# Kernel optimization log

Measured on AMD Instinct MI355X. Metric: run time of the kernel, lower is better.

## Reference

```python
import jax, jax.numpy as jnp
import numpy as np

N = 100_000      # nodes
E = 1_600_000    # edges (before self loops)
F_IN = 128       # dataset.num_node_features
H = 64           # hidden_channels
C = 10           # dataset.num_classes
B = 128          # graphs in batch
NEG_SLOPE = 0.2  # GATConv default


def setup_inputs() -> dict:
    key = jax.random.key(0)
    ks = jax.random.split(key, 16)
    s = 0.05
    x = jax.random.normal(ks[0], (N, F_IN), jnp.float32)
    edge_index = jax.random.randint(ks[1], (2, E), 0, N, dtype=jnp.int32).astype(jnp.int64)
    batch = jnp.sort(jax.random.randint(ks[2], (N,), 0, B, dtype=jnp.int32)).astype(jnp.int64)
    inp = {"x": x, "edge_index": edge_index, "batch": batch}
    # GATConv params: lin weight [out,in], att_src/att_dst [out], bias [out]
    dims = [(H, F_IN), (H, H), (H, H)]
    for i, (o, fi) in enumerate(dims, start=1):
        k = jax.random.split(ks[2 + i], 4)
        inp[f"W{i}"] = jax.random.normal(k[0], (o, fi), jnp.float32) * s
        inp[f"a_src{i}"] = jax.random.normal(k[1], (o,), jnp.float32) * s
        inp[f"a_dst{i}"] = jax.random.normal(k[2], (o,), jnp.float32) * s
        inp[f"b{i}"] = jax.random.normal(k[3], (o,), jnp.float32) * s
    inp["W_lin"] = jax.random.normal(ks[8], (C, H), jnp.float32) * s
    inp["b_lin"] = jax.random.normal(ks[9], (C,), jnp.float32) * s
    return inp


def gat_conv(x, src, dst, W, a_src, a_dst, b):
    # x: [N,Fin]; src/dst: [E+N] (self loops appended)
    h = x @ W.T                      # [N,H]
    e_src = h @ a_src                # [N] per-node src score
    e_dst = h @ a_dst                # [N] per-node dst score
    e = jax.nn.leaky_relu(e_src[src] + e_dst[dst], NEG_SLOPE)  # [E+N]
    # segment softmax over incoming edges of each dst node
    m = jax.ops.segment_max(e, dst, num_segments=N)
    ex = jnp.exp(e - m[dst])
    denom = jax.ops.segment_sum(ex, dst, num_segments=N)
    alpha = ex / denom[dst]          # [E+N]
    out = jax.ops.segment_sum(h[src] * alpha[:, None], dst, num_segments=N)
    return out + b


def reference(x, edge_index, batch, W1, a_src1, a_dst1, b1,
              W2, a_src2, a_dst2, b2, W3, a_src3, a_dst3, b3,
              W_lin, b_lin):
    loops = jnp.arange(N, dtype=edge_index.dtype)
    src = jnp.concatenate([edge_index[0], loops])
    dst = jnp.concatenate([edge_index[1], loops])
    h = jax.nn.relu(gat_conv(x, src, dst, W1, a_src1, a_dst1, b1))
    h = jax.nn.relu(gat_conv(h, src, dst, W2, a_src2, a_dst2, b2))
    h = gat_conv(h, src, dst, W3, a_src3, a_dst3, b3)
    # global mean pool over graphs
    sums = jax.ops.segment_sum(h, batch, num_segments=B)          # [B,H]
    cnt = jax.ops.segment_sum(jnp.ones((N,), h.dtype), batch, num_segments=B)
    pooled = sums / jnp.maximum(cnt, 1.0)[:, None]
    # dropout is identity in eval mode
    return pooled @ W_lin.T + b_lin   # [B,C]
```

## Files before the change

kernel.cpp:

```cpp
#include <hip/hip_runtime.h>
#include <hip/hip_bf16.h>

#define NN 100000
#define EE 1600000
#define ETOT 1700000
#define FIN1 128
#define HD 64
#define NC 10
#define NB 128
#define NEG 0.2f
#define LOG2E 1.44269504f

#define NBKT 196
#define BCAP 10240
#define BLKE 4096
#define ABLOCKS ((ETOT + BLKE - 1) / BLKE)
#define GBLOCKS ((NN + 63) / 64)


static constexpr size_t OFF_HA   = 0;
static constexpr size_t OFF_HB   = (size_t)NN * HD;
static constexpr size_t OFF_ESA  = (size_t)NN * HD * 2;
static constexpr size_t OFF_EDA  = OFF_ESA + (size_t)NN * 4;
static constexpr size_t OFF_ESB  = OFF_EDA + (size_t)NN * 4;
static constexpr size_t OFF_EDB  = OFF_ESB + (size_t)NN * 4;
static constexpr size_t OFF_ROW  = OFF_EDB + (size_t)NN * 4;
static constexpr size_t OFF_CSR  = OFF_ROW + (size_t)(NN + 4) * 4;
static constexpr size_t OFF_GC   = OFF_CSR + (size_t)ETOT * 4;
static constexpr size_t OFF_POOL = OFF_GC + 1024;
static constexpr size_t OFF_BKT  = OFF_POOL + (size_t)NB * HD * 4;

typedef __attribute__((ext_vector_type(8))) short short8;
typedef __attribute__((ext_vector_type(4))) float floatx4;
typedef __attribute__((ext_vector_type(2))) float floatx2;

__device__ __forceinline__ unsigned short f2bf(float f) {
  unsigned u = __float_as_uint(f);
  if ((u & 0x7F800000u) == 0x7F800000u) return (unsigned short)(u >> 16);
  return (unsigned short)((u + 0x7FFFu + ((u >> 16) & 1u)) >> 16);
}
__device__ __forceinline__ unsigned pk2(float a, float b) {
  return (unsigned)f2bf(a) | ((unsigned)f2bf(b) << 16);
}

#if __has_builtin(__builtin_amdgcn_cvt_pk_fp8_f32) && __has_builtin(__builtin_amdgcn_cvt_pk_f32_fp8)
#define HW_FP8 1
#endif
__device__ __forceinline__ unsigned enc1_fp8(float f) {
  _Float16 hf = (_Float16)f;
  unsigned short b = __builtin_bit_cast(unsigned short, hf);
  unsigned s = ((unsigned)b >> 8) & 0x80u;
  int mag = b & 0x7fff;
  if (mag < 0x2380) return s;
  int r = mag + 0x3F + ((mag >> 7) & 1);
  int m = (r >> 7) - 64;
  if (m > 0x7E) m = 0x7E;
  return s | (unsigned)m;
}
__device__ __forceinline__ unsigned pack4_fp8(float a, float b, float c, float d) {
#ifdef HW_FP8
  int w = __builtin_amdgcn_cvt_pk_fp8_f32(a, b, 0, false);
  w = __builtin_amdgcn_cvt_pk_fp8_f32(c, d, w, true);
  return (unsigned)w;
#else
  return enc1_fp8(a) | (enc1_fp8(b) << 8) | (enc1_fp8(c) << 16) | (enc1_fp8(d) << 24);
#endif
}
__device__ __forceinline__ float dec1_fp8(unsigned byte) {
  unsigned short hb = (unsigned short)(((byte & 0x80u) << 8) | ((byte & 0x7fu) << 7));
  _Float16 hf = __builtin_bit_cast(_Float16, hb);
  return (float)hf * 256.0f;
}
template <bool HI>
__device__ __forceinline__ floatx2 unpk2_fp8(unsigned w) {
#ifdef HW_FP8
  return __builtin_amdgcn_cvt_pk_f32_fp8((int)w, HI);
#else
  unsigned s = HI ? (w >> 16) : w;
  floatx2 r; r.x = dec1_fp8(s & 0xffu); r.y = dec1_fp8((s >> 8) & 0xffu);
  return r;
#endif
}

__device__ __forceinline__ void acc16(float* acc, float w, uint4 u) {
  floatx2 f0 = unpk2_fp8<false>(u.x), f1 = unpk2_fp8<true>(u.x);
  floatx2 f2 = unpk2_fp8<false>(u.y), f3 = unpk2_fp8<true>(u.y);
  floatx2 f4 = unpk2_fp8<false>(u.z), f5 = unpk2_fp8<true>(u.z);
  floatx2 f6 = unpk2_fp8<false>(u.w), f7 = unpk2_fp8<true>(u.w);
  acc[0]  = fmaf(w, f0.x, acc[0]);  acc[1]  = fmaf(w, f0.y, acc[1]);
  acc[2]  = fmaf(w, f1.x, acc[2]);  acc[3]  = fmaf(w, f1.y, acc[3]);
  acc[4]  = fmaf(w, f2.x, acc[4]);  acc[5]  = fmaf(w, f2.y, acc[5]);
  acc[6]  = fmaf(w, f3.x, acc[6]);  acc[7]  = fmaf(w, f3.y, acc[7]);
  acc[8]  = fmaf(w, f4.x, acc[8]);  acc[9]  = fmaf(w, f4.y, acc[9]);
  acc[10] = fmaf(w, f5.x, acc[10]); acc[11] = fmaf(w, f5.y, acc[11]);
  acc[12] = fmaf(w, f6.x, acc[12]); acc[13] = fmaf(w, f6.y, acc[13]);
  acc[14] = fmaf(w, f7.x, acc[14]); acc[15] = fmaf(w, f7.y, acc[15]);
}

__device__ __forceinline__ float aggregate_node(
    int n, int fl, const int* __restrict__ rowptr, const int* __restrict__ csr,
    const float* __restrict__ esIn, const float* __restrict__ edIn,
    const uint4* __restrict__ h16, float* acc) {
#pragma unroll
  for (int j = 0; j < 16; j++) acc[j] = 0.f;
  const float edn = edIn[n];
  const int row = rowptr[n];
  const int end = rowptr[n + 1];
  const int endm1 = end - 1;
  float den = 0.f;
  int idx0 = row + fl;
  int s_cur = csr[(idx0 < end) ? idx0 : endm1];
  float ev_cur = esIn[s_cur];
  for (int i = row; i < end; i += 4) {
    int inext = i + 4;
    int s_nxt = s_cur;
    if (inext < end) {
      int idn = inext + fl;
      s_nxt = csr[(idn < end) ? idn : endm1];
    }
    float ev_nxt = esIn[s_nxt];
    float e = ev_cur + edn;
    e = fmaxf(e, NEG * e);
    float w = exp2f(e);
    w = (i + fl < end) ? w : 0.f;
    den += w;
    int s0 = __shfl(s_cur, 0, 4), s1 = __shfl(s_cur, 1, 4);
    int s2 = __shfl(s_cur, 2, 4), s3 = __shfl(s_cur, 3, 4);
    float w0 = __shfl(w, 0, 4), w1 = __shfl(w, 1, 4);
    float w2 = __shfl(w, 2, 4), w3 = __shfl(w, 3, 4);
    uint4 u0 = h16[s0 * 4 + fl];
    uint4 u1 = h16[s1 * 4 + fl];
    uint4 u2 = h16[s2 * 4 + fl];
    uint4 u3 = h16[s3 * 4 + fl];
    acc16(acc, w0, u0);
    acc16(acc, w1, u1);
    acc16(acc, w2, u2);
    acc16(acc, w3, u3);
    s_cur = s_nxt;
    ev_cur = ev_nxt;
  }
  den += __shfl_xor(den, 1, 4);
  den += __shfl_xor(den, 2, 4);
  return 1.0f / den;
}

__device__ __forceinline__ void bucketA_body(
    int bid, const int* __restrict__ EI, unsigned* __restrict__ bucketed,
    int* __restrict__ gcur, char* smem) {
  unsigned* stage = (unsigned*)smem;
  unsigned short* sb = (unsigned short*)(smem + BLKE * 4);
  int* cnt  = (int*)(smem + BLKE * 4 + BLKE * 2);
  int* lofs = cnt + NBKT;
  int* base = lofs + NBKT;
  int* sc   = base + NBKT;
  const int t = threadIdx.x;
  const long long start = (long long)bid * BLKE;
  long long rem = (long long)ETOT - start;
  const int V = (rem < BLKE) ? (int)rem : BLKE;
  unsigned pk[BLKE / 256];
  short bk[BLKE / 256];
  for (int i = t; i < NBKT; i += 256) cnt[i] = 0;
  __syncthreads();
#pragma unroll
  for (int j = 0; j < BLKE / 256; j++) {
    long long k = start + t + 256 * j;
    bk[j] = -1;
    if (k < ETOT) {
      int s, d;
      if (k < EE) { s = EI[k]; d = EI[(long long)EE + k]; }
      else        { s = d = (int)(k - EE); }
      int b = d >> 9;
      pk[j] = ((unsigned)s << 9) | (unsigned)(d & 511);
      bk[j] = (short)b;
      atomicAdd(&cnt[b], 1);
    }
  }
  __syncthreads();
  int own = (t < NBKT) ? cnt[t] : 0;
  sc[t] = own;
  __syncthreads();
  for (int off = 1; off < 256; off <<= 1) {
    int add = (t >= off) ? sc[t - off] : 0;
    __syncthreads();
    sc[t] += add;
    __syncthreads();
  }
  if (t < NBKT) {
    lofs[t] = sc[t] - own;
    base[t] = (own > 0) ? atomicAdd(&gcur[t], own) : 0;
    cnt[t] = 0;
  }
  __syncthreads();
#pragma unroll
  for (int j = 0; j < BLKE / 256; j++) {
    if (bk[j] >= 0) {
      int b = bk[j];
      int p = lofs[b] + atomicAdd(&cnt[b], 1);
      stage[p] = pk[j];
      sb[p] = (unsigned short)b;
    }
  }
  __syncthreads();
  for (int i = t; i < V; i += 256) {
    int b = sb[i];
    int pos = base[b] + (i - lofs[b]);
    if (pos < BCAP) bucketed[(long long)b * BCAP + pos] = stage[i];
  }
}

__device__ __forceinline__ void gemm1_body(
    int bid, const float* __restrict__ X, const float* __restrict__ W,
    const float* __restrict__ As, const float* __restrict__ Ad,
    unsigned* __restrict__ hout, float* __restrict__ es, float* __restrict__ ed,
    char* smem) {
  constexpr int K = FIN1, RW = K / 2;
  unsigned* Xw = (unsigned*)smem;
  unsigned* Ww = (unsigned*)(smem + 16384);
  const int t = threadIdx.x;
  const int nodeBase = bid * 64;

  for (int i4 = t * 4; i4 < 64 * K; i4 += 1024) {
    int node = i4 >> 7, k = i4 & (K - 1);
    float4 v = make_float4(0.f, 0.f, 0.f, 0.f);
    if (nodeBase + node < NN)
      v = *(const float4*)(X + ((long long)(nodeBase + node) << 7) + k);
    uint2 p = make_uint2(pk2(v.x, v.y), pk2(v.z, v.w));
    int kw = k >> 1;
    *(uint2*)&Xw[node * RW + (kw ^ ((node & 7) << 2))] = p;
  }
  for (int i4 = t * 4; i4 < 64 * K; i4 += 1024) {
    int f = i4 >> 7, k = i4 & (K - 1);
    float4 v = *(const float4*)(W + ((long long)f << 7) + k);
    uint2 p = make_uint2(pk2(v.x, v.y), pk2(v.z, v.w));
    int kw = k >> 1;
    *(uint2*)&Ww[f * RW + (kw ^ ((f & 7) << 2))] = p;
  }
  __syncthreads();

  const int w = t >> 6, l = t & 63, m = l & 15, q = l >> 4;
  const int nodeLoc = 16 * w + m;
  const int sxa = (nodeLoc & 7) << 2;
  floatx4 acc[4];
#pragma unroll
  for (int nt = 0; nt < 4; nt++) acc[nt] = (floatx4){0.f, 0.f, 0.f, 0.f};
#pragma unroll
  for (int kc = 0; kc < K; kc += 32) {
    const int kcw = (kc >> 1) + 4 * q;
    short8 af = *(const short8*)&Xw[nodeLoc * RW + (kcw ^ sxa)];
#pragma unroll
    for (int nt = 0; nt < 4; nt++) {
      int f = 16 * nt + m;
      short8 bf = *(const short8*)&Ww[f * RW + (kcw ^ ((f & 7) << 2))];
      acc[nt] = __builtin_amdgcn_mfma_f32_16x16x32_bf16(af, bf, acc[nt], 0, 0, 0);
    }
  }
  float asv[4], adv[4];
#pragma unroll
  for (int nt = 0; nt < 4; nt++) { asv[nt] = As[16 * nt + m]; adv[nt] = Ad[16 * nt + m]; }
#pragma unroll
  for (int r = 0; r < 4; r++) {
    float ss = 0.f, sd2 = 0.f;
#pragma unroll
    for (int nt = 0; nt < 4; nt++) {
      ss = fmaf(acc[nt][r], asv[nt], ss);
      sd2 = fmaf(acc[nt][r], adv[nt], sd2);
    }
#pragma unroll
    for (int off = 1; off < 16; off <<= 1) {
      ss += __shfl_xor(ss, off);
      sd2 += __shfl_xor(sd2, off);
    }
    if (m == 0) {
      int gn = nodeBase + 16 * w + 4 * q + r;
      if (gn < NN) { es[gn] = ss * LOG2E; ed[gn] = sd2 * LOG2E; }
    }
  }
  {
    int gn = nodeBase + 16 * w + 4 * q;
#pragma unroll
    for (int nt = 0; nt < 4; nt++) {
#pragma unroll
      for (int r = 0; r < 4; r++) {
        float v = acc[nt][r];
        float p1 = __shfl_xor(v, 1);
        float p2 = __shfl_xor(v, 2);
        float p3 = __shfl_xor(v, 3);
        if ((m & 3) == 0 && (gn + r) < NN)
          hout[(gn + r) * 16 + 4 * nt + (m >> 2)] = pack4_fp8(v, p1, p2, p3);
      }
    }
  }
}

__global__ __launch_bounds__(256) void buildA_gemm1_kernel(
    const int* __restrict__ EI, unsigned* __restrict__ bucketed, int* __restrict__ gcur,
    const float* __restrict__ X, const float* __restrict__ W,
    const float* __restrict__ As, const float* __restrict__ Ad,
    unsigned* __restrict__ hout, float* __restrict__ es, float* __restrict__ ed) {
  __shared__ __align__(16) char smem[32768];
  if (blockIdx.x < ABLOCKS)
    bucketA_body(blockIdx.x, EI, bucketed, gcur, smem);
  else
    gemm1_body(blockIdx.x - ABLOCKS, X, W, As, Ad, hout, es, ed, smem);
}

__global__ __launch_bounds__(1024) void bucketB_kernel(
    const unsigned* __restrict__ bucketed, const int* __restrict__ gcur,
    int* __restrict__ rowptr, int* __restrict__ csr) {
  __shared__ int sc[256];
  __shared__ int hist[512];
  __shared__ int cur[512];
  __shared__ int ssum[256];
  const int t = threadIdx.x;
  const int b = blockIdx.x;
  if (t < 256) sc[t] = (t < NBKT) ? gcur[t] : 0;
  __syncthreads();
  for (int off = 1; off < 256; off <<= 1) {
    int add = (t >= off && t < 256) ? sc[t - off] : 0;
    __syncthreads();
    if (t < 256) sc[t] += add;
    __syncthreads();
  }
  const int cnt = gcur[b];
  const int base = sc[b] - cnt;
  if (b == 0 && t == 0) rowptr[NN] = ETOT;
  const unsigned* bp = bucketed + (long long)b * BCAP;
  if (t < 512) hist[t] = 0;
  __syncthreads();
  for (int i = t; i < cnt; i += 1024) atomicAdd(&hist[bp[i] & 511], 1);
  __syncthreads();
  int a0 = 0, a1 = 0, s = 0;
  if (t < 256) {
    a0 = hist[2 * t];
    a1 = hist[2 * t + 1];
    s = a0 + a1;
    ssum[t] = s;
  }
  __syncthreads();
  for (int off = 1; off < 256; off <<= 1) {
    int add = (t >= off && t < 256) ? ssum[t - off] : 0;
    __syncthreads();
    if (t < 256) ssum[t] += add;
    __syncthreads();
  }
  if (t < 256) {
    int ex = ssum[t] - s;
    cur[2 * t] = ex;
    cur[2 * t + 1] = ex + a0;
    int gn = b * 512 + 2 * t;
    if (gn < NN) rowptr[gn] = base + ex;
    if (gn + 1 < NN) rowptr[gn + 1] = base + ex + a0;
  }
  __syncthreads();
  for (int i = t; i < cnt; i += 1024) {
    unsigned e = bp[i];
    int pos = atomicAdd(&cur[e & 511], 1);
    csr[base + pos] = (int)(e >> 9);
  }
}

__global__ __launch_bounds__(256) void agg_gemm_kernel(
    const int* __restrict__ rowptr, const int* __restrict__ csr,
    const float* __restrict__ esIn, const float* __restrict__ edIn,
    const uint4* __restrict__ h16In, const float* __restrict__ biasA,
    const float* __restrict__ W, const float* __restrict__ As,
    const float* __restrict__ Ad,
    unsigned* __restrict__ hOut, float* __restrict__ esOut, float* __restrict__ edOut) {
  constexpr int K = HD, RW = K / 2;
  __shared__ unsigned Xw[64 * RW];
  __shared__ unsigned Ww[64 * RW];
  const int t = threadIdx.x;
  const int nodeBase = blockIdx.x * 64;

  for (int i4 = t * 4; i4 < 64 * K; i4 += 1024) {
    int f = i4 >> 6, k = i4 & (K - 1);
    float4 v = *(const float4*)(W + ((long long)f << 6) + k);
    uint2 p = make_uint2(pk2(v.x, v.y), pk2(v.z, v.w));
    int kw = k >> 1;
    *(uint2*)&Ww[f * RW + (kw ^ ((f & 7) << 2))] = p;
  }

  const int fl = t & 3;
  const int nl = t >> 2;
  const int n = nodeBase + nl;
  const int sxa = (nl & 7) << 2;
  const int wb0 = nl * RW + ((fl * 8) ^ sxa);
  const int wb1 = nl * RW + ((fl * 8 + 4) ^ sxa);
  if (n < NN) {
    float acc[16];
    const float inv = aggregate_node(n, fl, rowptr, csr, esIn, edIn, h16In, acc);
    float v[16];
#pragma unroll
    for (int j = 0; j < 16; j++)
      v[j] = fmaxf(acc[j] * inv + biasA[16 * fl + j], 0.f);
    uint4 pa, pb;
    pa.x = pk2(v[0], v[1]);   pa.y = pk2(v[2], v[3]);
    pa.z = pk2(v[4], v[5]);   pa.w = pk2(v[6], v[7]);
    pb.x = pk2(v[8], v[9]);   pb.y = pk2(v[10], v[11]);
    pb.z = pk2(v[12], v[13]); pb.w = pk2(v[14], v[15]);
    *(uint4*)&Xw[wb0] = pa;
    *(uint4*)&Xw[wb1] = pb;
  } else {
    *(uint4*)&Xw[wb0] = make_uint4(0u, 0u, 0u, 0u);
    *(uint4*)&Xw[wb1] = make_uint4(0u, 0u, 0u, 0u);
  }
  __syncthreads();

  const int w = t >> 6, l = t & 63, m = l & 15, q = l >> 4;
  const int nodeLoc = 16 * w + m;
  const int sxb = (nodeLoc & 7) << 2;
  floatx4 acc[4];
#pragma unroll
  for (int nt = 0; nt < 4; nt++) acc[nt] = (floatx4){0.f, 0.f, 0.f, 0.f};
#pragma unroll
  for (int kc = 0; kc < K; kc += 32) {
    const int kcw = (kc >> 1) + 4 * q;
    short8 af = *(const short8*)&Xw[nodeLoc * RW + (kcw ^ sxb)];
#pragma unroll
    for (int nt = 0; nt < 4; nt++) {
      int f = 16 * nt + m;
      short8 bf = *(const short8*)&Ww[f * RW + (kcw ^ ((f & 7) << 2))];
      acc[nt] = __builtin_amdgcn_mfma_f32_16x16x32_bf16(af, bf, acc[nt], 0, 0, 0);
    }
  }
  float asv[4], adv[4];
#pragma unroll
  for (int nt = 0; nt < 4; nt++) { asv[nt] = As[16 * nt + m]; adv[nt] = Ad[16 * nt + m]; }
#pragma unroll
  for (int r = 0; r < 4; r++) {
    float ss = 0.f, sd2 = 0.f;
#pragma unroll
    for (int nt = 0; nt < 4; nt++) {
      ss = fmaf(acc[nt][r], asv[nt], ss);
      sd2 = fmaf(acc[nt][r], adv[nt], sd2);
    }
#pragma unroll
    for (int off = 1; off < 16; off <<= 1) {
      ss += __shfl_xor(ss, off);
      sd2 += __shfl_xor(sd2, off);
    }
    if (m == 0) {
      int gn = nodeBase + 16 * w + 4 * q + r;
      if (gn < NN) { esOut[gn] = ss * LOG2E; edOut[gn] = sd2 * LOG2E; }
    }
  }
  {
    int gn = nodeBase + 16 * w + 4 * q;
#pragma unroll
    for (int nt = 0; nt < 4; nt++) {
#pragma unroll
      for (int r = 0; r < 4; r++) {
        float v = acc[nt][r];
        float p1 = __shfl_xor(v, 1);
        float p2 = __shfl_xor(v, 2);
        float p3 = __shfl_xor(v, 3);
        if ((m & 3) == 0 && (gn + r) < NN)
          hOut[(gn + r) * 16 + 4 * nt + (m >> 2)] = pack4_fp8(v, p1, p2, p3);
      }
    }
  }
}

__global__ __launch_bounds__(256) void agg3_pool_kernel(
    const int* __restrict__ rowptr, const int* __restrict__ csr,
    const float* __restrict__ esIn, const float* __restrict__ edIn,
    const uint4* __restrict__ h16In, const float* __restrict__ biasA,
    const int* __restrict__ batch, float* __restrict__ pooled) {
  __shared__ float P[64 * 66];
  __shared__ int gl[64];
  const int t = threadIdx.x;
  const int fl = t & 3;
  const int nl = t >> 2;
  const int n = blockIdx.x * 64 + nl;
  if (t < 64) {
    int bn = blockIdx.x * 64 + t;
    gl[t] = batch[(bn < NN) ? bn : (NN - 1)];
  }
  if (n < NN) {
    float acc[16];
    const float inv = aggregate_node(n, fl, rowptr, csr, esIn, edIn, h16In, acc);
#pragma unroll
    for (int j = 0; j < 16; j++)
      P[nl * 66 + 16 * fl + j] = acc[j] * inv + biasA[16 * fl + j];
  } else {
#pragma unroll
    for (int j = 0; j < 16; j++)
      P[nl * 66 + 16 * fl + j] = 0.f;
  }
  __syncthreads();
  if (t < HD) {
    const int f = t;
    float s = 0.f;
    int gcur = gl[0];
    for (int k = 0; k < 64; k++) {
      int g = gl[k];
      if (g != gcur) {
        atomicAdd(&pooled[gcur * HD + f], s);
        s = 0.f;
        gcur = g;
      }
      s += P[k * 66 + f];
    }
    atomicAdd(&pooled[gcur * HD + f], s);
  }
}

__device__ __forceinline__ int lower_bound_batch(const int* bt, int target) {
  int lo = 0, hi = NN;
  while (lo < hi) {
    int mid = (lo + hi) >> 1;
    if (bt[mid] < target) lo = mid + 1; else hi = mid;
  }
  return lo;
}

__global__ void final_kernel(
    const float* __restrict__ pooled, const int* __restrict__ batch,
    const float* __restrict__ Wlin, const float* __restrict__ blin,
    float* __restrict__ out) {
  int t = blockIdx.x * blockDim.x + threadIdx.x;
  if (t >= NB * NC) return;
  int b = t / NC, c = t - b * NC;
  int lo = lower_bound_batch(batch, b);
  int hi = lower_bound_batch(batch, b + 1);
  float inv = 1.0f / fmaxf((float)(hi - lo), 1.0f);
  float a = blin[c];
#pragma unroll 16
  for (int f = 0; f < HD; f++)
    a = fmaf(pooled[b * HD + f] * inv, Wlin[(long long)c * HD + f], a);
  out[t] = a;
}

extern "C" void kernel_launch(void* const* d_in, const int* in_sizes, int n_in,
                              void* d_out, int out_size, void* d_ws, size_t ws_size,
                              hipStream_t stream) {
  char* ws = (char*)d_ws;
  unsigned* hA       = (unsigned*)(ws + OFF_HA);
  unsigned* hB       = (unsigned*)(ws + OFF_HB);
  float*    esA      = (float*)(ws + OFF_ESA);
  float*    edA      = (float*)(ws + OFF_EDA);
  float*    esB      = (float*)(ws + OFF_ESB);
  float*    edB      = (float*)(ws + OFF_EDB);
  int*      rowptr   = (int*)(ws + OFF_ROW);
  int*      csr      = (int*)(ws + OFF_CSR);
  int*      gcur     = (int*)(ws + OFF_GC);
  float*    pooled   = (float*)(ws + OFF_POOL);
  unsigned* bucketed = (unsigned*)(ws + OFF_BKT);

  const float* X  = (const float*)d_in[0];
  const int*   EI = (const int*)d_in[1];
  const int*   BT = (const int*)d_in[2];
  const float* Wm[3] = {(const float*)d_in[3], (const float*)d_in[7], (const float*)d_in[11]};
  const float* As[3] = {(const float*)d_in[4], (const float*)d_in[8], (const float*)d_in[12]};
  const float* Ad[3] = {(const float*)d_in[5], (const float*)d_in[9], (const float*)d_in[13]};
  const float* Bb[3] = {(const float*)d_in[6], (const float*)d_in[10], (const float*)d_in[14]};
  const float* Wl = (const float*)d_in[15];
  const float* bl = (const float*)d_in[16];

  (void)hipMemsetAsync(gcur, 0, 1024 + (size_t)NB * HD * 4, stream);
  buildA_gemm1_kernel<<<ABLOCKS + GBLOCKS, 256, 0, stream>>>(
      EI, bucketed, gcur, X, Wm[0], As[0], Ad[0], hA, esA, edA);
  bucketB_kernel<<<NBKT, 1024, 0, stream>>>(bucketed, gcur, rowptr, csr);
  agg_gemm_kernel<<<GBLOCKS, 256, 0, stream>>>(
      rowptr, csr, esA, edA, (const uint4*)hA, Bb[0],
      Wm[1], As[1], Ad[1], hB, esB, edB);
  agg_gemm_kernel<<<GBLOCKS, 256, 0, stream>>>(
      rowptr, csr, esB, edB, (const uint4*)hB, Bb[1],
      Wm[2], As[2], Ad[2], hA, esA, edA);
  agg3_pool_kernel<<<GBLOCKS, 256, 0, stream>>>(
      rowptr, csr, esA, edA, (const uint4*)hA, Bb[2], BT, pooled);
  final_kernel<<<(NB * NC + 255) / 256, 256, 0, stream>>>(pooled, BT, Wl, bl, (float*)d_out);
}
```

Baseline: 286.3 us.

## Balance edge aggregation across threads with flat edge-range split and LDS atomics

Replaces per-node aggregation (one 4-lane group per destination node) with a flat split of the block's contiguous CSR edge range evenly across the 64 lane groups. Each group finds its starting destination by binary search over a shared rowptr copy, accumulates weighted features, and flushes partial sums and softmax denominators into shared memory with atomics whenever the destination changes. This targets load imbalance from varying node in-degrees within a wavefront. In exchange it adds LDS atomic traffic and extra synchronization, and the layer-3 pooling buffer drops its row padding.

```diff
diff --git a/kernel.cpp b/kernel.cpp
--- a/kernel.cpp
+++ b/kernel.cpp
@@ -97,51 +97,92 @@
   acc[14] = fmaf(w, f7.x, acc[14]); acc[15] = fmaf(w, f7.y, acc[15]);
 }
 
-__device__ __forceinline__ float aggregate_node(
-    int n, int fl, const int* __restrict__ rowptr, const int* __restrict__ csr,
-    const float* __restrict__ esIn, const float* __restrict__ edIn,
-    const uint4* __restrict__ h16, float* acc) {
+__device__ __forceinline__ void flushP(float* P, float* den, float* acc,
+                                       float& wsum, int dcur, int fl) {
+  if (dcur >= 0) {
+    int base = dcur * 64 + 16 * fl;
+#pragma unroll
+    for (int j = 0; j < 16; j++) { atomicAdd(&P[base + j], acc[j]); acc[j] = 0.f; }
+    if (fl == 0) atomicAdd(&den[dcur], wsum);
+    wsum = 0.f;
+  }
+}
+
+#define CONS(pj, wj, uj) { int dj = (pj) & 63;                        \
+    if (dj != dcur) { flushP(P, den, acc, wsum, dcur, fl); dcur = dj; } \
+    wsum += (wj); acc16(acc, (wj), (uj)); }
+
+__device__ __forceinline__ void flat_agg(
+    int t, const int* __restrict__ csr, const float* __restrict__ esIn,
+    const uint4* __restrict__ h16, const int* rowLds, const float* edLds,
+    float* P, float* den) {
+  const int fl = t & 3;
+  const int g = t >> 2;
+  const int e0 = rowLds[0];
+  const int total = rowLds[64] - e0;
+  const int gbeg = e0 + ((total * g) >> 6);
+  const int gend = e0 + ((total * (g + 1)) >> 6);
+  const int nit = (gend - gbeg + 3) >> 2;
+  float acc[16];
 #pragma unroll
   for (int j = 0; j < 16; j++) acc[j] = 0.f;
-  const float edn = edIn[n];
-  const int row = rowptr[n];
-  const int end = rowptr[n + 1];
-  const int endm1 = end - 1;
-  float den = 0.f;
-  int idx0 = row + fl;
-  int s_cur = csr[(idx0 < end) ? idx0 : endm1];
-  float ev_cur = esIn[s_cur];
-  for (int i = row; i < end; i += 4) {
-    int inext = i + 4;
-    int s_nxt = s_cur;
-    if (inext < end) {
-      int idn = inext + fl;
-      s_nxt = csr[(idn < end) ? idn : endm1];
-    }
-    float ev_nxt = esIn[s_nxt];
-    float e = ev_cur + edn;
-    e = fmaxf(e, NEG * e);
-    float w = exp2f(e);
-    w = (i + fl < end) ? w : 0.f;
-    den += w;
-    int s0 = __shfl(s_cur, 0, 4), s1 = __shfl(s_cur, 1, 4);
-    int s2 = __shfl(s_cur, 2, 4), s3 = __shfl(s_cur, 3, 4);
-    float w0 = __shfl(w, 0, 4), w1 = __shfl(w, 1, 4);
-    float w2 = __shfl(w, 2, 4), w3 = __shfl(w, 3, 4);
-    uint4 u0 = h16[s0 * 4 + fl];
-    uint4 u1 = h16[s1 * 4 + fl];
-    uint4 u2 = h16[s2 * 4 + fl];
-    uint4 u3 = h16[s3 * 4 + fl];
-    acc16(acc, w0, u0);
-    acc16(acc, w1, u1);
-    acc16(acc, w2, u2);
-    acc16(acc, w3, u3);
-    s_cur = s_nxt;
-    ev_cur = ev_nxt;
-  }
-  den += __shfl_xor(den, 1, 4);
-  den += __shfl_xor(den, 2, 4);
-  return 1.0f / den;
+  float wsum = 0.f;
+  int dcur = -1;
+
+  int idx = gbeg + fl;
+  int idxc = (idx < gend) ? idx : (gend - 1);
+  int d;
+  {
+    int lo = 0, hi = 63;
+#pragma unroll
+    for (int stp = 0; stp < 6; stp++) {
+      int mid = (lo + hi + 1) >> 1;
+      if (rowLds[mid] <= idxc) lo = mid; else hi = mid - 1;
+    }
+    d = lo;
+  }
+  int s = csr[idxc];
+  float e = esIn[s] + edLds[d];
+  e = fmaxf(e, NEG * e);
+  float wOwn = (idx < gend) ? exp2f(e) : 0.f;
+  int packOwn = (s << 6) | d;
+
+  int p0 = __shfl(packOwn, 0, 4), p1 = __shfl(packOwn, 1, 4);
+  int p2 = __shfl(packOwn, 2, 4), p3 = __shfl(packOwn, 3, 4);
+  float w0 = __shfl(wOwn, 0, 4), w1 = __shfl(wOwn, 1, 4);
+  float w2 = __shfl(wOwn, 2, 4), w3 = __shfl(wOwn, 3, 4);
+  uint4 u0 = h16[(p0 >> 6) * 4 + fl];
+  uint4 u1 = h16[(p1 >> 6) * 4 + fl];
+  uint4 u2 = h16[(p2 >> 6) * 4 + fl];
+  uint4 u3 = h16[(p3 >> 6) * 4 + fl];
+
+  for (int it = 1; it <= nit; it++) {
+    if (it < nit) {
+      idx = gbeg + 4 * it + fl;
+      idxc = (idx < gend) ? idx : (gend - 1);
+      while (idxc >= rowLds[d + 1]) d++;
+      s = csr[idxc];
+      float e2 = esIn[s] + edLds[d];
+      e2 = fmaxf(e2, NEG * e2);
+      wOwn = (idx < gend) ? exp2f(e2) : 0.f;
+      packOwn = (s << 6) | d;
+      int q0 = __shfl(packOwn, 0, 4), q1 = __shfl(packOwn, 1, 4);
+      int q2 = __shfl(packOwn, 2, 4), q3 = __shfl(packOwn, 3, 4);
+      float x0 = __shfl(wOwn, 0, 4), x1 = __shfl(wOwn, 1, 4);
+      float x2 = __shfl(wOwn, 2, 4), x3 = __shfl(wOwn, 3, 4);
+      uint4 v0 = h16[(q0 >> 6) * 4 + fl];
+      uint4 v1 = h16[(q1 >> 6) * 4 + fl];
+      uint4 v2 = h16[(q2 >> 6) * 4 + fl];
+      uint4 v3 = h16[(q3 >> 6) * 4 + fl];
+      CONS(p0, w0, u0) CONS(p1, w1, u1) CONS(p2, w2, u2) CONS(p3, w3, u3)
+      p0 = q0; p1 = q1; p2 = q2; p3 = q3;
+      w0 = x0; w1 = x1; w2 = x2; w3 = x3;
+      u0 = v0; u1 = v1; u2 = v2; u3 = v3;
+    } else {
+      CONS(p0, w0, u0) CONS(p1, w1, u1) CONS(p2, w2, u2) CONS(p3, w3, u3)
+    }
+  }
+  flushP(P, den, acc, wsum, dcur, fl);
 }
 
 __device__ __forceinline__ void bucketA_body(
@@ -366,43 +407,65 @@
     const float* __restrict__ W, const float* __restrict__ As,
     const float* __restrict__ Ad,
     unsigned* __restrict__ hOut, float* __restrict__ esOut, float* __restrict__ edOut) {
-  constexpr int K = HD, RW = K / 2;
-  __shared__ unsigned Xw[64 * RW];
+  constexpr int RW = 32;
+  __shared__ __align__(16) float P[64 * 64];
+  __shared__ float den[64];
   __shared__ unsigned Ww[64 * RW];
+  __shared__ int rowLds[65];
+  __shared__ float edLds[64];
+  unsigned* Xw = (unsigned*)P;
   const int t = threadIdx.x;
   const int nodeBase = blockIdx.x * 64;
 
-  for (int i4 = t * 4; i4 < 64 * K; i4 += 1024) {
-    int f = i4 >> 6, k = i4 & (K - 1);
+  for (int i4 = t * 4; i4 < 64 * 64; i4 += 1024) {
+    int f = i4 >> 6, k = i4 & 63;
     float4 v = *(const float4*)(W + ((long long)f << 6) + k);
     uint2 p = make_uint2(pk2(v.x, v.y), pk2(v.z, v.w));
     int kw = k >> 1;
     *(uint2*)&Ww[f * RW + (kw ^ ((f & 7) << 2))] = p;
   }
-
-  const int fl = t & 3;
-  const int nl = t >> 2;
-  const int n = nodeBase + nl;
-  const int sxa = (nl & 7) << 2;
-  const int wb0 = nl * RW + ((fl * 8) ^ sxa);
-  const int wb1 = nl * RW + ((fl * 8 + 4) ^ sxa);
-  if (n < NN) {
-    float acc[16];
-    const float inv = aggregate_node(n, fl, rowptr, csr, esIn, edIn, h16In, acc);
-    float v[16];
-#pragma unroll
-    for (int j = 0; j < 16; j++)
-      v[j] = fmaxf(acc[j] * inv + biasA[16 * fl + j], 0.f);
-    uint4 pa, pb;
-    pa.x = pk2(v[0], v[1]);   pa.y = pk2(v[2], v[3]);
-    pa.z = pk2(v[4], v[5]);   pa.w = pk2(v[6], v[7]);
-    pb.x = pk2(v[8], v[9]);   pb.y = pk2(v[10], v[11]);
-    pb.z = pk2(v[12], v[13]); pb.w = pk2(v[14], v[15]);
-    *(uint4*)&Xw[wb0] = pa;
-    *(uint4*)&Xw[wb1] = pb;
-  } else {
-    *(uint4*)&Xw[wb0] = make_uint4(0u, 0u, 0u, 0u);
-    *(uint4*)&Xw[wb1] = make_uint4(0u, 0u, 0u, 0u);
+  if (t < 65) rowLds[t] = rowptr[(nodeBase + t < NN) ? (nodeBase + t) : NN];
+  if (t < 64) {
+    int n = nodeBase + t;
+    edLds[t] = (n < NN) ? edIn[n] : 0.f;
+    den[t] = 0.f;
+  }
+  {
+    float4 z = make_float4(0.f, 0.f, 0.f, 0.f);
+    float4* P4 = (float4*)P;
+#pragma unroll
+    for (int j = 0; j < 4; j++) P4[t * 4 + j] = z;
+  }
+  __syncthreads();
+
+  flat_agg(t, csr, esIn, h16In, rowLds, edLds, P, den);
+  __syncthreads();
+
+  const int fb = t & 3;
+  const int n2 = t >> 2;
+  float v[16];
+  {
+    float dd = den[n2];
+    float inv = (dd > 0.f) ? 1.0f / dd : 0.f;
+    const bool valid = (nodeBase + n2) < NN;
+    float av[16];
+#pragma unroll
+    for (int j = 0; j < 16; j++) av[j] = P[n2 * 64 + fb * 16 + j];
+#pragma unroll
+    for (int j = 0; j < 16; j++) {
+      float x = fmaxf(fmaf(av[j], inv, biasA[fb * 16 + j]), 0.f);
+      v[j] = valid ? x : 0.f;
+    }
+  }
+  __syncthreads();
+  {
+    const int sxa = (n2 & 7) << 2;
+    const int wb0 = n2 * RW + ((fb * 8) ^ sxa);
+    const int wb1 = n2 * RW + ((fb * 8 + 4) ^ sxa);
+    *(uint4*)&Xw[wb0] = make_uint4(pk2(v[0], v[1]), pk2(v[2], v[3]),
+                                   pk2(v[4], v[5]), pk2(v[6], v[7]));
+    *(uint4*)&Xw[wb1] = make_uint4(pk2(v[8], v[9]), pk2(v[10], v[11]),
+                                   pk2(v[12], v[13]), pk2(v[14], v[15]));
   }
   __syncthreads();
 
@@ -413,7 +476,7 @@
 #pragma unroll
   for (int nt = 0; nt < 4; nt++) acc[nt] = (floatx4){0.f, 0.f, 0.f, 0.f};
 #pragma unroll
-  for (int kc = 0; kc < K; kc += 32) {
+  for (int kc = 0; kc < HD; kc += 32) {
     const int kcw = (kc >> 1) + 4 * q;
     short8 af = *(const short8*)&Xw[nodeLoc * RW + (kcw ^ sxb)];
 #pragma unroll
@@ -450,12 +513,12 @@
     for (int nt = 0; nt < 4; nt++) {
 #pragma unroll
       for (int r = 0; r < 4; r++) {
-        float v = acc[nt][r];
-        float p1 = __shfl_xor(v, 1);
-        float p2 = __shfl_xor(v, 2);
-        float p3 = __shfl_xor(v, 3);
+        float vv = acc[nt][r];
+        float p1 = __shfl_xor(vv, 1);
+        float p2 = __shfl_xor(vv, 2);
+        float p3 = __shfl_xor(vv, 3);
         if ((m & 3) == 0 && (gn + r) < NN)
-          hOut[(gn + r) * 16 + 4 * nt + (m >> 2)] = pack4_fp8(v, p1, p2, p3);
+          hOut[(gn + r) * 16 + 4 * nt + (m >> 2)] = pack4_fp8(vv, p1, p2, p3);
       }
     }
   }
@@ -466,26 +529,42 @@
     const float* __restrict__ esIn, const float* __restrict__ edIn,
     const uint4* __restrict__ h16In, const float* __restrict__ biasA,
     const int* __restrict__ batch, float* __restrict__ pooled) {
-  __shared__ float P[64 * 66];
+  __shared__ __align__(16) float P[64 * 64];
+  __shared__ float den[64];
+  __shared__ int rowLds[65];
+  __shared__ float edLds[64];
   __shared__ int gl[64];
   const int t = threadIdx.x;
-  const int fl = t & 3;
-  const int nl = t >> 2;
-  const int n = blockIdx.x * 64 + nl;
+  const int nodeBase = blockIdx.x * 64;
+  if (t < 65) rowLds[t] = rowptr[(nodeBase + t < NN) ? (nodeBase + t) : NN];
   if (t < 64) {
-    int bn = blockIdx.x * 64 + t;
-    gl[t] = batch[(bn < NN) ? bn : (NN - 1)];
-  }
-  if (n < NN) {
-    float acc[16];
-    const float inv = aggregate_node(n, fl, rowptr, csr, esIn, edIn, h16In, acc);
-#pragma unroll
-    for (int j = 0; j < 16; j++)
-      P[nl * 66 + 16 * fl + j] = acc[j] * inv + biasA[16 * fl + j];
-  } else {
-#pragma unroll
-    for (int j = 0; j < 16; j++)
-      P[nl * 66 + 16 * fl + j] = 0.f;
+    int n = nodeBase + t;
+    edLds[t] = (n < NN) ? edIn[n] : 0.f;
+    den[t] = 0.f;
+    gl[t] = batch[(n < NN) ? n : (NN - 1)];
+  }
+  {
+    float4 z = make_float4(0.f, 0.f, 0.f, 0.f);
+    float4* P4 = (float4*)P;
+#pragma unroll
+    for (int j = 0; j < 4; j++) P4[t * 4 + j] = z;
+  }
+  __syncthreads();
+
+  flat_agg(t, csr, esIn, h16In, rowLds, edLds, P, den);
+  __syncthreads();
+
+  {
+    const int fb = t & 3;
+    const int n2 = t >> 2;
+    float dd = den[n2];
+    float inv = (dd > 0.f) ? 1.0f / dd : 0.f;
+    const bool valid = (nodeBase + n2) < NN;
+#pragma unroll
+    for (int j = 0; j < 16; j++) {
+      float x = fmaf(P[n2 * 64 + fb * 16 + j], inv, biasA[fb * 16 + j]);
+      P[n2 * 64 + fb * 16 + j] = valid ? x : 0.f;
+    }
   }
   __syncthreads();
   if (t < HD) {
@@ -499,7 +578,7 @@
         s = 0.f;
         gcur = g;
       }
-      s += P[k * 66 + f];
+      s += P[k * 64 + f];
     }
     atomicAdd(&pooled[gcur * HD + f], s);
   }
```

Measured after the change: 451.9 us. +57.8%, slower.
